# Kernel optimization log

Measured on AMD Instinct MI355X. Metric: run time of the kernel, lower is better.

The kernel has to match this reference:

```python
import jax, jax.numpy as jnp
import numpy as np

B, T, I, H, L = 64, 512, 256, 1024, 4


def _uniform(key, shape, fan):
    # matches torch nn.RNN/Linear init: U(-1/sqrt(fan), 1/sqrt(fan))
    bound = 1.0 / np.sqrt(fan)
    return jax.random.uniform(key, shape, jnp.float32, -bound, bound)


def setup_inputs() -> dict:
    key = jax.random.key(0)
    keys = jax.random.split(key, 32)
    inp = {"x": jax.random.normal(keys[0], (B, T, I), jnp.float32)}
    k = 1
    for l in range(L):
        din = I if l == 0 else H
        inp[f"W_ih{l}"] = _uniform(keys[k], (H, din), H); k += 1
        inp[f"W_hh{l}"] = _uniform(keys[k], (H, H), H); k += 1
        inp[f"b_ih{l}"] = _uniform(keys[k], (H,), H); k += 1
        inp[f"b_hh{l}"] = _uniform(keys[k], (H,), H); k += 1
    inp["fc_w"] = _uniform(keys[k], (1, H), H); k += 1
    inp["fc_b"] = _uniform(keys[k], (1,), H)
    return inp


def _rnn_layer(x_seq, W_ih, b_ih, W_hh, b_hh):
    # x_seq: [B, T, Din] -> hidden states [B, T, H]
    # Precompute the input projection for all timesteps in one big GEMM.
    xW = jnp.einsum('btd,hd->bth', x_seq, W_ih) + b_ih  # [B, T, H]

    def step(h, xw_t):
        # h_t = tanh(W_ih x_t + b_ih + W_hh h_{t-1} + b_hh)
        h_new = jnp.tanh(xw_t + h @ W_hh.T + b_hh)
        return h_new, h_new

    h0 = jnp.zeros((x_seq.shape[0], W_hh.shape[0]), x_seq.dtype)
    _, hs = jax.lax.scan(step, h0, jnp.swapaxes(xW, 0, 1))  # [T, B, H]
    return jnp.swapaxes(hs, 0, 1)  # [B, T, H]


def reference(x,
              W_ih0, W_hh0, b_ih0, b_hh0,
              W_ih1, W_hh1, b_ih1, b_hh1,
              W_ih2, W_hh2, b_ih2, b_hh2,
              W_ih3, W_hh3, b_ih3, b_hh3,
              fc_w, fc_b):
    h = x
    layer_params = [
        (W_ih0, b_ih0, W_hh0, b_hh0),
        (W_ih1, b_ih1, W_hh1, b_hh1),
        (W_ih2, b_ih2, W_hh2, b_hh2),
        (W_ih3, b_ih3, W_hh3, b_hh3),
    ]
    for (W_ih, b_ih, W_hh, b_hh) in layer_params:
        h = _rnn_layer(h, W_ih, b_ih, W_hh, b_hh)
    return h @ fc_w.T + fc_b  # [B, T, 1]
```

## Files before the change

### kernel.cpp

```cpp
#include <hip/hip_runtime.h>


typedef _Float16 f16;
typedef _Float16 f16x8 __attribute__((ext_vector_type(8)));
typedef float    f32x4 __attribute__((ext_vector_type(4)));

#define BB 64
#define TT 512
#define II 256
#define HH 1024
#define RING 64

union U16u { unsigned long long u[2]; f16x8 v; };

#define SYS_LOAD_U64(p) __hip_atomic_load((const unsigned long long*)(p), \
    __ATOMIC_RELAXED, __HIP_MEMORY_SCOPE_SYSTEM)
#define SYS_STORE_U64(p, x) __hip_atomic_store((unsigned long long*)(p), (x), \
    __ATOMIC_RELAXED, __HIP_MEMORY_SCOPE_SYSTEM)

#define MFMA(a, b, c) __builtin_amdgcn_mfma_f32_16x16x32_f16((a), (b), (c), 0, 0, 0)

__global__ __launch_bounds__(256) void cvt_kernel(const float* __restrict__ in,
                                                  f16* __restrict__ out, int n4) {
  int stride = gridDim.x * blockDim.x;
  for (int i = blockIdx.x * blockDim.x + threadIdx.x; i < n4; i += stride) {
    float4 v = reinterpret_cast<const float4*>(in)[i];
    _Float16 __attribute__((ext_vector_type(4))) h = { (f16)v.x, (f16)v.y,
                                                       (f16)v.z, (f16)v.w };
    reinterpret_cast<decltype(h)*>(out)[i] = h;
  }
}

__global__ __launch_bounds__(256) void bsum_kernel(const float* __restrict__ a,
                                                   const float* __restrict__ b,
                                                   float* __restrict__ o) {
  int i = blockIdx.x * blockDim.x + threadIdx.x;
  if (i < HH) o[i] = a[i] + b[i];
}

__global__ __launch_bounds__(256) void zero_kernel(int* __restrict__ p, int n) {
  int i = blockIdx.x * blockDim.x + threadIdx.x;
  if (i < n) p[i] = 0;
}

__global__ __launch_bounds__(256) void initout_kernel(float* __restrict__ out,
                                                      const float* __restrict__ fcb,
                                                      int n) {
  int i = blockIdx.x * blockDim.x + threadIdx.x;
  if (i < n) out[i] = fcb[0];
}

__global__ __launch_bounds__(256, 1) void rnn_persist(
    const float* __restrict__ x,
    f16* __restrict__ ring0, f16* __restrict__ ring1,
    f16* __restrict__ ring2, f16* __restrict__ ring3,
    const f16* __restrict__ wih0, const f16* __restrict__ wih1,
    const f16* __restrict__ wih2, const f16* __restrict__ wih3,
    const f16* __restrict__ whh0, const f16* __restrict__ whh1,
    const f16* __restrict__ whh2, const f16* __restrict__ whh3,
    const float* __restrict__ bs0, const float* __restrict__ bs1,
    const float* __restrict__ bs2, const float* __restrict__ bs3,
    const float* __restrict__ fcw, float* __restrict__ out,
    int* __restrict__ flags) {
  const int p = blockIdx.x & 15, wgp = blockIdx.x >> 4;
  const int l = p >> 2, bg = p & 3;
  const int wave = threadIdx.x >> 6, lane = threadIdx.x & 63;
  const int l15 = lane & 15, quad = lane >> 4;
  const int b0 = bg * 16, r0 = wgp * 64;
  const int srow = threadIdx.x >> 4;
  const int scol = (threadIdx.x & 15) * 4;

  __shared__ f32x4 red[16 * 64];
  __shared__ __align__(16) f16 hstage[16 * 64];

  f16* rings[4] = { ring0, ring1, ring2, ring3 };
  const f16* wih_t[4] = { wih0, wih1, wih2, wih3 };
  const f16* whh_t[4] = { whh0, whh1, whh2, whh3 };
  const float* bs_t[4] = { bs0, bs1, bs2, bs3 };

  const f16* in_ring = (l > 0) ? rings[l - 1] : (const f16*)0;
  f16* out_ring = rings[l];
  const float bv = bs_t[l][r0 + wave * 16 + l15];

  f16x8 whhF[4][8];
  {
    const f16* q = whh_t[l] + (size_t)(r0 + l15) * HH + wave * 256 + quad * 8;
#pragma unroll
    for (int j = 0; j < 4; ++j)
#pragma unroll
      for (int f = 0; f < 8; ++f)
        whhF[j][f] = *reinterpret_cast<const f16x8*>(q + (size_t)j * 16 * HH + f * 32);
  }
  f16x8 wihF[4][8];
  if (l == 0) {
    const f16* q = wih0 + (size_t)(r0 + l15) * II + wave * 64 + quad * 8;
#pragma unroll
    for (int j = 0; j < 4; ++j)
#pragma unroll
      for (int f = 0; f < 2; ++f)
        wihF[j][f] = *reinterpret_cast<const f16x8*>(q + (size_t)j * 16 * II + f * 32);
  } else {
    const f16* q = wih_t[l] + (size_t)(r0 + l15) * HH + wave * 256 + quad * 8;
#pragma unroll
    for (int j = 0; j < 4; ++j)
#pragma unroll
      for (int f = 0; f < 8; ++f)
        wihF[j][f] = *reinterpret_cast<const f16x8*>(q + (size_t)j * 16 * HH + f * 32);
  }
  float4 fcwv = { 0.f, 0.f, 0.f, 0.f };
  if (l == 3) fcwv = *reinterpret_cast<const float4*>(fcw + r0 + (threadIdx.x & 15) * 4);

  const int which = lane >> 4;
  int psel = p + (which == 1 ? -4 : which == 2 ? 4 : 0);
  psel = psel < 0 ? 0 : (psel > 15 ? 15 : psel);
  const int* fptr = flags + (psel * 16 + l15) * 16;
  unsigned long long needA = 0;
  if (l > 0) needA |= 0xFFFF0000ull;
  if (l < 3) needA |= 0xFFFF00000000ull;
  int* myflag = flags + (p * 16 + wgp) * 16;

  for (int t = 0; t < TT; ++t) {
    const int slot = t & (RING - 1);
    f32x4 c0 = {}, c1 = {}, c2 = {}, c3 = {};

    if (wave == 0 && needA && (l > 0 || t >= RING)) {
      const int tgtA = (which == 1) ? t + 1 : t - RING + 1;
      const bool part = (which == 1 && l > 0) || (which == 2 && l < 3);
      for (;;) {
        int v = part ? __hip_atomic_load(fptr, __ATOMIC_RELAXED,
                                         __HIP_MEMORY_SCOPE_SYSTEM)
                     : 0x7FFFFFFF;
        if ((__ballot(v >= tgtA) & needA) == needA) break;
      }
    }
    if (l > 0) __syncthreads();

    if (l == 0) {
      const float* xp = x + ((size_t)(b0 + l15) * TT + t) * II + wave * 64 + quad * 8;
#pragma unroll
      for (int f = 0; f < 2; ++f) {
        float4 u0 = *reinterpret_cast<const float4*>(xp + f * 32);
        float4 u1 = *reinterpret_cast<const float4*>(xp + f * 32 + 4);
        f16x8 a = { (f16)u0.x, (f16)u0.y, (f16)u0.z, (f16)u0.w,
                    (f16)u1.x, (f16)u1.y, (f16)u1.z, (f16)u1.w };
        c0 = MFMA(a, wihF[0][f], c0);
        c1 = MFMA(a, wihF[1][f], c1);
        c2 = MFMA(a, wihF[2][f], c2);
        c3 = MFMA(a, wihF[3][f], c3);
      }
    } else {
      const char* ip = (const char*)(in_ring + ((size_t)(b0 + l15) * RING + slot) * HH +
                                     wave * 256 + quad * 8);
#pragma unroll
      for (int f = 0; f < 8; ++f) {
        U16u av;
        av.u[0] = SYS_LOAD_U64(ip + f * 64);
        av.u[1] = SYS_LOAD_U64(ip + f * 64 + 8);
        c0 = MFMA(av.v, wihF[0][f], c0);
        c1 = MFMA(av.v, wihF[1][f], c1);
        c2 = MFMA(av.v, wihF[2][f], c2);
        c3 = MFMA(av.v, wihF[3][f], c3);
      }
    }

    if (t > 0) {
      if (wave == 0) {
        for (;;) {
          int v = (which == 0) ? __hip_atomic_load(fptr, __ATOMIC_RELAXED,
                                                   __HIP_MEMORY_SCOPE_SYSTEM)
                               : 0x7FFFFFFF;
          if ((__ballot(v >= t) & 0xFFFFull) == 0xFFFFull) break;
        }
      }
      __syncthreads();

      const int slotp = (t - 1) & (RING - 1);
      const char* hp = (const char*)(out_ring + ((size_t)(b0 + l15) * RING + slotp) * HH +
                                     wave * 256 + quad * 8);
#pragma unroll
      for (int f = 0; f < 8; ++f) {
        U16u av;
        av.u[0] = SYS_LOAD_U64(hp + f * 64);
        av.u[1] = SYS_LOAD_U64(hp + f * 64 + 8);
        c0 = MFMA(av.v, whhF[0][f], c0);
        c1 = MFMA(av.v, whhF[1][f], c1);
        c2 = MFMA(av.v, whhF[2][f], c2);
        c3 = MFMA(av.v, whhF[3][f], c3);
      }
    }

    red[(wave * 4 + 0) * 64 + lane] = c0;
    red[(wave * 4 + 1) * 64 + lane] = c1;
    red[(wave * 4 + 2) * 64 + lane] = c2;
    red[(wave * 4 + 3) * 64 + lane] = c3;
    __syncthreads();
    f32x4 tot = red[(0 * 4 + wave) * 64 + lane] + red[(1 * 4 + wave) * 64 + lane] +
                red[(2 * 4 + wave) * 64 + lane] + red[(3 * 4 + wave) * 64 + lane];

#pragma unroll
    for (int i = 0; i < 4; ++i) {
      float e = __expf(2.0f * (tot[i] + bv));
      hstage[(quad * 4 + i) * 64 + wave * 16 + l15] = (f16)(1.0f - 2.0f / (e + 1.0f));
    }
    __syncthreads();

    unsigned long long hw =
        *reinterpret_cast<const unsigned long long*>(&hstage[srow * 64 + scol]);
    SYS_STORE_U64(out_ring + ((size_t)(b0 + srow) * RING + slot) * HH + r0 + scol, hw);

    if (l == 3) {
      union { unsigned long long u; f16 h[4]; } hu;
      hu.u = hw;
      float partial = (float)hu.h[0] * fcwv.x + (float)hu.h[1] * fcwv.y +
                      (float)hu.h[2] * fcwv.z + (float)hu.h[3] * fcwv.w;
      partial += __shfl_down(partial, 8, 16);
      partial += __shfl_down(partial, 4, 16);
      partial += __shfl_down(partial, 2, 16);
      partial += __shfl_down(partial, 1, 16);
      if ((threadIdx.x & 15) == 0)
        atomicAdd(out + (size_t)(b0 + srow) * TT + t, partial);
    }

    asm volatile("s_waitcnt vmcnt(0)" ::: "memory");
    __syncthreads();
    if (threadIdx.x == 0)
      __hip_atomic_store(myflag, t + 1, __ATOMIC_RELAXED, __HIP_MEMORY_SCOPE_SYSTEM);
  }
}

extern "C" void kernel_launch(void* const* d_in, const int* in_sizes, int n_in,
                              void* d_out, int out_size, void* d_ws, size_t ws_size,
                              hipStream_t stream) {
  const float* x   = (const float*)d_in[0];
  const float* fcw = (const float*)d_in[17];
  const float* fcb = (const float*)d_in[18];

  char* ws = (char*)d_ws;
  size_t off = 0;
  auto alloc = [&](size_t bytes) -> void* {
    void* p = ws + off;
    off += (bytes + 255) & ~(size_t)255;
    return p;
  };
  f16* ring[4];
  for (int l = 0; l < 4; ++l)
    ring[l] = (f16*)alloc((size_t)BB * RING * HH * 2);
  f16* w16ih[4];
  f16* w16hh[4];
  float* bsum[4];
  for (int l = 0; l < 4; ++l) {
    int din = (l == 0) ? II : HH;
    w16ih[l] = (f16*)alloc((size_t)HH * din * 2);
    w16hh[l] = (f16*)alloc((size_t)HH * HH * 2);
    bsum[l]  = (float*)alloc(HH * 4);
  }
  int* flags = (int*)alloc(256 * 16 * 4);

  for (int l = 0; l < 4; ++l) {
    int din = (l == 0) ? II : HH;
    cvt_kernel<<<512, 256, 0, stream>>>((const float*)d_in[1 + 4 * l], w16ih[l],
                                        HH * din / 4);
    cvt_kernel<<<512, 256, 0, stream>>>((const float*)d_in[2 + 4 * l], w16hh[l],
                                        HH * HH / 4);
    bsum_kernel<<<4, 256, 0, stream>>>((const float*)d_in[3 + 4 * l],
                                       (const float*)d_in[4 + 4 * l], bsum[l]);
  }
  zero_kernel<<<16, 256, 0, stream>>>(flags, 256 * 16);
  initout_kernel<<<BB * TT / 256, 256, 0, stream>>>((float*)d_out, fcb, BB * TT);

  rnn_persist<<<256, 256, 0, stream>>>(
      x, ring[0], ring[1], ring[2], ring[3],
      w16ih[0], w16ih[1], w16ih[2], w16ih[3],
      w16hh[0], w16hh[1], w16hh[2], w16hh[3],
      bsum[0], bsum[1], bsum[2], bsum[3],
      fcw, (float*)d_out, flags);
}
```

Before: 3.321 ms.

## Split recurrent handoff into XCC-local fast path with L2-scoped loads and flags

Adds a startup census that reads each workgroup's XCC id so every group of 16 partner blocks learns whether they share an XCC. The recurrent hidden-state exchange moves into a small double-buffered per-group buffer with its own flag array. When the group is co-located it uses sc0 (L2-scope) loads and stores instead of system-scope atomics. Cross-layer handoff now uses a separate system flag array, published earlier, and caches the last observed flag value to skip polling. This targets per-step latency on the serial recurrence but depends on the block-to-XCC placement and adds extra stores and barriers.

After: 3.043 ms. 1.09x faster.

```diff
diff --git a/kernel.cpp b/kernel.cpp
--- a/kernel.cpp
+++ b/kernel.cpp
@@ -17,8 +17,35 @@
     __ATOMIC_RELAXED, __HIP_MEMORY_SCOPE_SYSTEM)
 #define SYS_STORE_U64(p, x) __hip_atomic_store((unsigned long long*)(p), (x), \
     __ATOMIC_RELAXED, __HIP_MEMORY_SCOPE_SYSTEM)
+#define SYS_LOAD_I32(p) __hip_atomic_load((const int*)(p), \
+    __ATOMIC_RELAXED, __HIP_MEMORY_SCOPE_SYSTEM)
+#define SYS_STORE_I32(p, x) __hip_atomic_store((int*)(p), (x), \
+    __ATOMIC_RELAXED, __HIP_MEMORY_SCOPE_SYSTEM)
 
 #define MFMA(a, b, c) __builtin_amdgcn_mfma_f32_16x16x32_f16((a), (b), (c), 0, 0, 0)
+
+__device__ __forceinline__ void l2_load_u64(unsigned long long& d, const void* p) {
+  asm volatile("global_load_dwordx2 %0, %1, off sc0" : "=v"(d) : "v"(p) : "memory");
+}
+__device__ __forceinline__ void l2_store_u64(void* p, unsigned long long v) {
+  asm volatile("global_store_dwordx2 %0, %1, off sc0" :: "v"(p), "v"(v) : "memory");
+}
+__device__ __forceinline__ int l2_load_flag(const void* p) {
+  int v;
+  asm volatile("global_load_dword %0, %1, off sc0\n\ts_waitcnt vmcnt(0)"
+               : "=v"(v) : "v"(p) : "memory");
+  return v;
+}
+__device__ __forceinline__ void l2_store_flag(void* p, int v) {
+  asm volatile("global_store_dword %0, %1, off sc0" :: "v"(p), "v"(v) : "memory");
+}
+__device__ __forceinline__ void waitcnt0() {
+  asm volatile("s_waitcnt vmcnt(0)" ::: "memory");
+}
+#define TIE16(b) asm volatile("s_waitcnt vmcnt(0)" \
+  : "+v"(b[0]), "+v"(b[1]), "+v"(b[2]), "+v"(b[3]), "+v"(b[4]), "+v"(b[5]), \
+    "+v"(b[6]), "+v"(b[7]), "+v"(b[8]), "+v"(b[9]), "+v"(b[10]), "+v"(b[11]), \
+    "+v"(b[12]), "+v"(b[13]), "+v"(b[14]), "+v"(b[15]) :: "memory")
 
 __global__ __launch_bounds__(256) void cvt_kernel(const float* __restrict__ in,
                                                   f16* __restrict__ out, int n4) {
@@ -52,8 +79,8 @@
 
 __global__ __launch_bounds__(256, 1) void rnn_persist(
     const float* __restrict__ x,
-    f16* __restrict__ ring0, f16* __restrict__ ring1,
-    f16* __restrict__ ring2, f16* __restrict__ ring3,
+    f16* __restrict__ ring0, f16* __restrict__ ring1, f16* __restrict__ ring2,
+    f16* __restrict__ hfastg,
     const f16* __restrict__ wih0, const f16* __restrict__ wih1,
     const f16* __restrict__ wih2, const f16* __restrict__ wih3,
     const f16* __restrict__ whh0, const f16* __restrict__ whh1,
@@ -61,7 +88,8 @@
     const float* __restrict__ bs0, const float* __restrict__ bs1,
     const float* __restrict__ bs2, const float* __restrict__ bs3,
     const float* __restrict__ fcw, float* __restrict__ out,
-    int* __restrict__ flags) {
+    int* __restrict__ flag_fast, int* __restrict__ flag_sys,
+    int* __restrict__ census) {
   const int p = blockIdx.x & 15, wgp = blockIdx.x >> 4;
   const int l = p >> 2, bg = p & 3;
   const int wave = threadIdx.x >> 6, lane = threadIdx.x & 63;
@@ -72,14 +100,34 @@
 
   __shared__ f32x4 red[16 * 64];
   __shared__ __align__(16) f16 hstage[16 * 64];
-
-  f16* rings[4] = { ring0, ring1, ring2, ring3 };
+  __shared__ int sfast;
+
+  {
+    int xcc;
+    asm volatile("s_getreg_b32 %0, hwreg(HW_REG_XCC_ID)" : "=s"(xcc));
+    if (threadIdx.x == 0) SYS_STORE_I32(&census[p * 16 + wgp], xcc + 1);
+    if (wave == 0) {
+      int v = 1;
+      for (;;) {
+        v = (lane < 16) ? SYS_LOAD_I32(&census[p * 16 + lane]) : 1;
+        if (__all(v != 0)) break;
+      }
+      int v0 = __shfl(v, 0, 64);
+      int eq = __all((lane < 16) ? (v == v0) : 1);
+      if (lane == 0) sfast = eq;
+    }
+    __syncthreads();
+  }
+  const bool fast = (sfast != 0);
+
+  f16* rings[4] = { ring0, ring1, ring2, (f16*)0 };
   const f16* wih_t[4] = { wih0, wih1, wih2, wih3 };
   const f16* whh_t[4] = { whh0, whh1, whh2, whh3 };
   const float* bs_t[4] = { bs0, bs1, bs2, bs3 };
 
   const f16* in_ring = (l > 0) ? rings[l - 1] : (const f16*)0;
   f16* out_ring = rings[l];
+  f16* hfast = hfastg + (size_t)p * 2 * 16 * HH;
   const float bv = bs_t[l][r0 + wave * 16 + l15];
 
   f16x8 whhF[4][8];
@@ -113,27 +161,33 @@
   const int which = lane >> 4;
   int psel = p + (which == 1 ? -4 : which == 2 ? 4 : 0);
   psel = psel < 0 ? 0 : (psel > 15 ? 15 : psel);
-  const int* fptr = flags + (psel * 16 + l15) * 16;
+  const int* fsysp = flag_sys + (psel * 16 + l15) * 16;
+  const int* ffastp = flag_fast + (p * 16 + l15) * 16;
   unsigned long long needA = 0;
   if (l > 0) needA |= 0xFFFF0000ull;
   if (l < 3) needA |= 0xFFFF00000000ull;
-  int* myflag = flags + (p * 16 + wgp) * 16;
+  int* myff = flag_fast + (p * 16 + wgp) * 16;
+  int* myfs = flag_sys + (p * 16 + wgp) * 16;
+  const bool partA = (which == 1 && l > 0) || (which == 2 && l < 3);
+  int pvA = 0;
 
   for (int t = 0; t < TT; ++t) {
     const int slot = t & (RING - 1);
+
+    if (wave == 0 && needA && (l > 0 || t + 1 >= RING)) {
+      const int tgtA = (which == 1) ? t + 1 : t - RING + 1;
+      int v = partA ? pvA : 0x7FFFFFFF;
+      if ((__ballot(v >= tgtA) & needA) != needA) {
+        for (;;) {
+          v = partA ? SYS_LOAD_I32(fsysp) : 0x7FFFFFFF;
+          if ((__ballot(v >= tgtA) & needA) == needA) break;
+        }
+      }
+      pvA = partA ? SYS_LOAD_I32(fsysp) : 0x7FFFFFFF;
+    }
+    if (l > 0) __syncthreads();
+
     f32x4 c0 = {}, c1 = {}, c2 = {}, c3 = {};
-
-    if (wave == 0 && needA && (l > 0 || t >= RING)) {
-      const int tgtA = (which == 1) ? t + 1 : t - RING + 1;
-      const bool part = (which == 1 && l > 0) || (which == 2 && l < 3);
-      for (;;) {
-        int v = part ? __hip_atomic_load(fptr, __ATOMIC_RELAXED,
-                                         __HIP_MEMORY_SCOPE_SYSTEM)
-                     : 0x7FFFFFFF;
-        if ((__ballot(v >= tgtA) & needA) == needA) break;
-      }
-    }
-    if (l > 0) __syncthreads();
 
     if (l == 0) {
       const float* xp = x + ((size_t)(b0 + l15) * TT + t) * II + wave * 64 + quad * 8;
@@ -164,24 +218,49 @@
     }
 
     if (t > 0) {
+      waitcnt0();
+      __syncthreads();
+      if (threadIdx.x == 0) SYS_STORE_I32(myfs, t);
+    }
+
+    if (t > 0) {
       if (wave == 0) {
-        for (;;) {
-          int v = (which == 0) ? __hip_atomic_load(fptr, __ATOMIC_RELAXED,
-                                                   __HIP_MEMORY_SCOPE_SYSTEM)
-                               : 0x7FFFFFFF;
-          if ((__ballot(v >= t) & 0xFFFFull) == 0xFFFFull) break;
+        if (fast) {
+          for (;;) {
+            int v = (which == 0) ? l2_load_flag(ffastp) : 0x7FFFFFFF;
+            if ((__ballot(v >= t) & 0xFFFFull) == 0xFFFFull) break;
+          }
+        } else {
+          for (;;) {
+            int v = (which == 0) ? SYS_LOAD_I32(ffastp) : 0x7FFFFFFF;
+            if ((__ballot(v >= t) & 0xFFFFull) == 0xFFFFull) break;
+          }
         }
       }
       __syncthreads();
 
-      const int slotp = (t - 1) & (RING - 1);
-      const char* hp = (const char*)(out_ring + ((size_t)(b0 + l15) * RING + slotp) * HH +
-                                     wave * 256 + quad * 8);
+      unsigned long long hbuf[16];
+      const char* hp = (const char*)(hfast + (size_t)((t - 1) & 1) * 16 * HH +
+                                     (size_t)l15 * HH + wave * 256 + quad * 8);
+      if (fast) {
+#pragma unroll
+        for (int f = 0; f < 8; ++f) {
+          l2_load_u64(hbuf[2 * f], hp + f * 64);
+          l2_load_u64(hbuf[2 * f + 1], hp + f * 64 + 8);
+        }
+        TIE16(hbuf);
+      } else {
+#pragma unroll
+        for (int f = 0; f < 8; ++f) {
+          hbuf[2 * f] = SYS_LOAD_U64(hp + f * 64);
+          hbuf[2 * f + 1] = SYS_LOAD_U64(hp + f * 64 + 8);
+        }
+      }
 #pragma unroll
       for (int f = 0; f < 8; ++f) {
         U16u av;
-        av.u[0] = SYS_LOAD_U64(hp + f * 64);
-        av.u[1] = SYS_LOAD_U64(hp + f * 64 + 8);
+        av.u[0] = hbuf[2 * f];
+        av.u[1] = hbuf[2 * f + 1];
         c0 = MFMA(av.v, whhF[0][f], c0);
         c1 = MFMA(av.v, whhF[1][f], c1);
         c2 = MFMA(av.v, whhF[2][f], c2);
@@ -206,9 +285,21 @@
 
     unsigned long long hw =
         *reinterpret_cast<const unsigned long long*>(&hstage[srow * 64 + scol]);
-    SYS_STORE_U64(out_ring + ((size_t)(b0 + srow) * RING + slot) * HH + r0 + scol, hw);
-
-    if (l == 3) {
+    {
+      void* dst = hfast + (size_t)(t & 1) * 16 * HH + (size_t)srow * HH + r0 + scol;
+      if (fast) l2_store_u64(dst, hw);
+      else      SYS_STORE_U64(dst, hw);
+    }
+    waitcnt0();
+    __syncthreads();
+    if (threadIdx.x == 0) {
+      if (fast) l2_store_flag(myff, t + 1);
+      else      SYS_STORE_I32(myff, t + 1);
+    }
+
+    if (l < 3) {
+      SYS_STORE_U64(out_ring + ((size_t)(b0 + srow) * RING + slot) * HH + r0 + scol, hw);
+    } else {
       union { unsigned long long u; f16 h[4]; } hu;
       hu.u = hw;
       float partial = (float)hu.h[0] * fcwv.x + (float)hu.h[1] * fcwv.y +
@@ -220,12 +311,11 @@
       if ((threadIdx.x & 15) == 0)
         atomicAdd(out + (size_t)(b0 + srow) * TT + t, partial);
     }
-
-    asm volatile("s_waitcnt vmcnt(0)" ::: "memory");
-    __syncthreads();
-    if (threadIdx.x == 0)
-      __hip_atomic_store(myflag, t + 1, __ATOMIC_RELAXED, __HIP_MEMORY_SCOPE_SYSTEM);
-  }
+  }
+
+  waitcnt0();
+  __syncthreads();
+  if (threadIdx.x == 0) SYS_STORE_I32(myfs, TT);
 }
 
 extern "C" void kernel_launch(void* const* d_in, const int* in_sizes, int n_in,
@@ -242,9 +332,10 @@
     off += (bytes + 255) & ~(size_t)255;
     return p;
   };
-  f16* ring[4];
-  for (int l = 0; l < 4; ++l)
+  f16* ring[3];
+  for (int l = 0; l < 3; ++l)
     ring[l] = (f16*)alloc((size_t)BB * RING * HH * 2);
+  f16* hfast = (f16*)alloc((size_t)16 * 2 * 16 * HH * 2);
   f16* w16ih[4];
   f16* w16hh[4];
   float* bsum[4];
@@ -254,7 +345,9 @@
     w16hh[l] = (f16*)alloc((size_t)HH * HH * 2);
     bsum[l]  = (float*)alloc(HH * 4);
   }
-  int* flags = (int*)alloc(256 * 16 * 4);
+  int* flag_fast = (int*)alloc(256 * 16 * 4);
+  int* flag_sys  = (int*)alloc(256 * 16 * 4);
+  int* census    = (int*)alloc(256 * 4);
 
   for (int l = 0; l < 4; ++l) {
     int din = (l == 0) ? II : HH;
@@ -265,13 +358,15 @@
     bsum_kernel<<<4, 256, 0, stream>>>((const float*)d_in[3 + 4 * l],
                                        (const float*)d_in[4 + 4 * l], bsum[l]);
   }
-  zero_kernel<<<16, 256, 0, stream>>>(flags, 256 * 16);
+  zero_kernel<<<17, 256, 0, stream>>>(flag_fast, 256 * 16);
+  zero_kernel<<<17, 256, 0, stream>>>(flag_sys, 256 * 16);
+  zero_kernel<<<1, 256, 0, stream>>>(census, 256);
   initout_kernel<<<BB * TT / 256, 256, 0, stream>>>((float*)d_out, fcb, BB * TT);
 
   rnn_persist<<<256, 256, 0, stream>>>(
-      x, ring[0], ring[1], ring[2], ring[3],
+      x, ring[0], ring[1], ring[2], hfast,
       w16ih[0], w16ih[1], w16ih[2], w16ih[3],
       w16hh[0], w16hh[1], w16hh[2], w16hh[3],
       bsum[0], bsum[1], bsum[2], bsum[3],
-      fcw, (float*)d_out, flags);
-}
+      fcw, (float*)d_out, flag_fast, flag_sys, census);
+}
```
